# Optimization experiments

Hardware: AMD Instinct MI355X
Metric: run time of the kernel (lower is better)

The kernel has to match this reference:

```python
import jax, jax.numpy as jnp
import numpy as np

D = 1024  # input_size == context_size

def setup_inputs() -> dict:
    key = jax.random.key(0)
    ks = jax.random.split(key, 8)
    B, S = 16, 4096
    s = 1.0 / np.sqrt(D)
    return {
        "x": jax.random.normal(ks[0], (B, S, D), dtype=jnp.float32),
        "context": jax.random.normal(ks[1], (B, D), dtype=jnp.float32),
        "W_in": jax.random.uniform(ks[2], (D, D), jnp.float32, -s, s),
        "b_in": jax.random.uniform(ks[3], (D,), jnp.float32, -s, s),
        "W_ctx": jax.random.uniform(ks[4], (D, D), jnp.float32, -s, s),
        "b_ctx": jax.random.uniform(ks[5], (D,), jnp.float32, -s, s),
        "w_att": jax.random.uniform(ks[6], (D,), jnp.float32, -s, s),
        "b_att": jax.random.uniform(ks[7], (), jnp.float32, -s, s),
    }

def reference(x, context, W_in, b_in, W_ctx, b_ctx, w_att, b_att):
    # projected_input: [B,S,D]; projected_context: [B,D] broadcast over S
    pi = jnp.einsum('bsd,ed->bse', x, W_in) + b_in
    pc = jnp.einsum('bd,ed->be', context, W_ctx) + b_ctx
    h = jnp.tanh(pi + pc[:, None, :])                      # [B,S,D]
    scores = jnp.einsum('bsd,d->bs', h, w_att) + b_att      # [B,S]
    weights = jax.nn.softmax(scores, axis=1)                # [B,S]
    context_vector = jnp.einsum('bs,bsd->bd', weights, x)   # [B,D]
    # dropout is identity in eval mode
    return context_vector
```

## Files before the change

kernel.cpp:

```cpp
#include <hip/hip_runtime.h>
#include <hip/hip_bf16.h>
#include <math.h>

#define NB 16
#define NS 4096
#define ND 1024
#define NM (NB * NS)

#define WS_T       0
#define WS_SCORES  16384
#define WS_WEIGHTS (WS_SCORES + NB * NS)
#define WS_SHARED  (WS_WEIGHTS + NB * NS)
#define WS_XBF16   (WS_SHARED + 524288)
#define WS_SPART   (WS_XBF16 + 33554432)
#define WS_NEED    (((size_t)WS_SPART + 524288) * 4)

typedef short v8s __attribute__((ext_vector_type(8)));
typedef float v4f __attribute__((ext_vector_type(4)));
typedef unsigned short ushort;

#define G_AS __attribute__((address_space(1)))
#define L_AS __attribute__((address_space(3)))

__device__ __forceinline__ ushort f2bf(float f) {
    __hip_bfloat16 h = __float2bfloat16(f);
    return *reinterpret_cast<ushort*>(&h);
}

__device__ __forceinline__ float bf2f(ushort u) {
    return __uint_as_float(((unsigned)u) << 16);
}

__device__ __forceinline__ float fast_tanh(float x) {
    float e = __expf(2.0f * x);
    return 1.0f - 2.0f / (e + 1.0f);
}

__global__ __launch_bounds__(256) void convw_kernel(const float* __restrict__ W,
                                                    ushort* __restrict__ Wb) {
    int flat = blockIdx.x * 256 + threadIdx.x;
#pragma unroll
    for (int j = 0; j < 2; ++j) {
        int idx = flat + j * 131072;
        float4 v = ((const float4*)W)[idx];
        ushort4 o;
        o.x = f2bf(v.x); o.y = f2bf(v.y); o.z = f2bf(v.z); o.w = f2bf(v.w);
        ((ushort4*)Wb)[idx] = o;
    }
}

__global__ __launch_bounds__(256) void convx_kernel(const float* __restrict__ x,
                                                    ushort* __restrict__ xb) {
    size_t base = (size_t)blockIdx.x * 256 + threadIdx.x;
#pragma unroll
    for (int i = 0; i < 16; ++i) {
        size_t idx8 = base + (size_t)i * 524288;
        float4 a = ((const float4*)x)[idx8 * 2];
        float4 c = ((const float4*)x)[idx8 * 2 + 1];
        v8s o;
        o[0] = (short)f2bf(a.x); o[1] = (short)f2bf(a.y);
        o[2] = (short)f2bf(a.z); o[3] = (short)f2bf(a.w);
        o[4] = (short)f2bf(c.x); o[5] = (short)f2bf(c.y);
        o[6] = (short)f2bf(c.z); o[7] = (short)f2bf(c.w);
        ((v8s*)xb)[idx8] = o;
    }
}

__global__ __launch_bounds__(256) void tvec_kernel(const float* __restrict__ context,
                                                   const float* __restrict__ W_ctx,
                                                   const float* __restrict__ b_in,
                                                   const float* __restrict__ b_ctx,
                                                   float* __restrict__ t) {
    __shared__ float ctx[ND];
    int b = blockIdx.y;
    int tid = threadIdx.x;
    for (int i = tid; i < ND; i += 256) ctx[i] = context[b * ND + i];
    __syncthreads();
    int e = blockIdx.x * 64 + (tid >> 2);
    int kq = tid & 3;
    const float4* wr = (const float4*)(W_ctx + (size_t)e * ND + kq * 256);
    const float4* cr = (const float4*)(ctx + kq * 256);
    float acc = 0.f;
#pragma unroll 4
    for (int k = 0; k < 64; ++k) {
        float4 w = wr[k];
        float4 c = cr[k];
        acc += c.x * w.x + c.y * w.y + c.z * w.z + c.w * w.w;
    }
    acc += __shfl_xor(acc, 1);
    acc += __shfl_xor(acc, 2);
    if (kq == 0) t[b * ND + e] = acc + b_in[e] + b_ctx[e];
}

__global__ __launch_bounds__(256) void scores_tile_kernel(const ushort* __restrict__ xbf,
                                                          const ushort* __restrict__ Wb,
                                                          const float* __restrict__ t,
                                                          const float* __restrict__ w_att,
                                                          float* __restrict__ spart) {
    __shared__ ushort As[2][4096];
    __shared__ ushort Bs[2][4096];
    __shared__ float red[4][64];

    int tid = threadIdx.x;
    int o = blockIdx.x;
    int rt = (o & 7) * 64 + (o >> 6);
    int ct = (o >> 3) & 7;
    int row0 = rt << 7;
    int e0 = ct << 7;
    int b = row0 >> 12;

    int g0 = tid, g1 = tid + 256;
    const ushort* gaA0 = xbf + (size_t)(row0 + (g0 >> 2)) * ND + (g0 & 3) * 8;
    const ushort* gaA1 = xbf + (size_t)(row0 + (g1 >> 2)) * ND + (g1 & 3) * 8;
    const ushort* gaB0 = Wb  + (size_t)(e0  + (g0 >> 2)) * ND + (g0 & 3) * 8;
    const ushort* gaB1 = Wb  + (size_t)(e0  + (g1 >> 2)) * ND + (g1 & 3) * 8;

    __builtin_amdgcn_global_load_lds((const G_AS void*)gaA0, (L_AS void*)&As[0][g0 * 8], 16, 0, 0);
    __builtin_amdgcn_global_load_lds((const G_AS void*)gaA1, (L_AS void*)&As[0][g1 * 8], 16, 0, 0);
    __builtin_amdgcn_global_load_lds((const G_AS void*)gaB0, (L_AS void*)&Bs[0][g0 * 8], 16, 0, 0);
    __builtin_amdgcn_global_load_lds((const G_AS void*)gaB1, (L_AS void*)&Bs[0][g1 * 8], 16, 0, 0);
    __syncthreads();

    int w = tid >> 6, l = tid & 63;
    int l15 = l & 15, kq4 = l >> 4;
    int R = (w >> 1) * 64;
    int E = (w & 1) * 64;

    v4f acc[4][4];
#pragma unroll
    for (int i = 0; i < 4; ++i)
#pragma unroll
        for (int j = 0; j < 4; ++j) acc[i][j] = (v4f)(0.f);

#pragma unroll 2
    for (int kt = 0; kt < 32; ++kt) {
        int bi = kt & 1;
        if (kt < 31) {
            int ko = (kt + 1) * 32;
            __builtin_amdgcn_global_load_lds((const G_AS void*)(gaA0 + ko), (L_AS void*)&As[bi ^ 1][g0 * 8], 16, 0, 0);
            __builtin_amdgcn_global_load_lds((const G_AS void*)(gaA1 + ko), (L_AS void*)&As[bi ^ 1][g1 * 8], 16, 0, 0);
            __builtin_amdgcn_global_load_lds((const G_AS void*)(gaB0 + ko), (L_AS void*)&Bs[bi ^ 1][g0 * 8], 16, 0, 0);
            __builtin_amdgcn_global_load_lds((const G_AS void*)(gaB1 + ko), (L_AS void*)&Bs[bi ^ 1][g1 * 8], 16, 0, 0);
        }
        v8s af[4], bf[4];
#pragma unroll
        for (int mf = 0; mf < 4; ++mf)
            af[mf] = *(const v8s*)&As[bi][((R + mf * 16 + l15) * 4 + kq4) * 8];
#pragma unroll
        for (int nf = 0; nf < 4; ++nf)
            bf[nf] = *(const v8s*)&Bs[bi][((E + nf * 16 + l15) * 4 + kq4) * 8];
#pragma unroll
        for (int mf = 0; mf < 4; ++mf)
#pragma unroll
            for (int nf = 0; nf < 4; ++nf)
                acc[mf][nf] = __builtin_amdgcn_mfma_f32_16x16x32_bf16(
                    af[mf], bf[nf], acc[mf][nf], 0, 0, 0);
        __syncthreads();
    }

    float s[4][4];
#pragma unroll
    for (int i = 0; i < 4; ++i)
#pragma unroll
        for (int j = 0; j < 4; ++j) s[i][j] = 0.f;

#pragma unroll
    for (int nf = 0; nf < 4; ++nf) {
        int e = e0 + E + nf * 16 + l15;
        float tv = t[b * ND + e];
        float wv = w_att[e];
#pragma unroll
        for (int mf = 0; mf < 4; ++mf)
#pragma unroll
            for (int r = 0; r < 4; ++r)
                s[mf][r] += fast_tanh(acc[mf][nf][r] + tv) * wv;
    }
#pragma unroll
    for (int mf = 0; mf < 4; ++mf)
#pragma unroll
        for (int r = 0; r < 4; ++r) {
            float v = s[mf][r];
            v += __shfl_xor(v, 1);
            v += __shfl_xor(v, 2);
            v += __shfl_xor(v, 4);
            v += __shfl_xor(v, 8);
            s[mf][r] = v;
        }
    if (l15 == 0) {
#pragma unroll
        for (int mf = 0; mf < 4; ++mf)
#pragma unroll
            for (int r = 0; r < 4; ++r)
                red[w][mf * 16 + kq4 * 4 + r] = s[mf][r];
    }
    __syncthreads();
    if (tid < 128) {
        int half = tid >> 6;
        int rl = tid & 63;
        float v = red[half * 2][rl] + red[half * 2 + 1][rl];
        spart[ct * 65536 + row0 + half * 64 + rl] = v;
    }
}

__global__ __launch_bounds__(512) void scores_mfma_kernel(const float* __restrict__ x,
                                                          const ushort* __restrict__ Wb,
                                                          const float* __restrict__ t,
                                                          const float* __restrict__ w_att,
                                                          float* __restrict__ scores) {
    __shared__ ushort As[2][64 * 256];
    __shared__ float red[8][64];

    int tid = threadIdx.x;
    int row0 = blockIdx.x * 64;
    int b = row0 >> 12;
    const float4* xf4 = (const float4*)x;

    int sr = tid >> 3;
    int sc = tid & 7;
    int swzbase = (sr & 7) << 3;

    float4 nx[8];
#pragma unroll
    for (int j = 0; j < 8; ++j)
        nx[j] = xf4[(size_t)(row0 + sr) * 256 + sc + j * 8];
#pragma unroll
    for (int j = 0; j < 8; ++j) {
        int c4 = sc + j * 8;
        ushort4 o;
        o.x = f2bf(nx[j].x); o.y = f2bf(nx[j].y); o.z = f2bf(nx[j].z); o.w = f2bf(nx[j].w);
        *(ushort4*)&As[0][sr * 256 + ((c4 * 4) ^ swzbase)] = o;
    }
    __syncthreads();

    int w = tid >> 6;
    int l = tid & 63;
    int l15 = l & 15;
    int kofs = (l >> 4) * 8;
    int xorv = (l & 7) << 3;
    int n0 = w * 128;

    v4f acc[2][4][4];
#pragma unroll
    for (int p = 0; p < 2; ++p)
#pragma unroll
        for (int i = 0; i < 4; ++i)
#pragma unroll
            for (int j = 0; j < 4; ++j) acc[p][i][j] = (v4f)(0.f);

    const ushort* bbase0 = Wb + (size_t)(n0 + l15) * ND + kofs;
    const ushort* bbase1 = bbase0 + (size_t)64 * ND;

#pragma unroll
    for (int kh = 0; kh < 4; ++kh) {
        if (kh < 3) {
#pragma unroll
            for (int j = 0; j < 8; ++j)
                nx[j] = xf4[(size_t)(row0 + sr) * 256 + (kh + 1) * 64 + sc + j * 8];
        }
        const ushort* Ab = &As[kh & 1][0];
        int kb = kh * 256;

        v8s b0c[4], b0n[4], b1[4];
#pragma unroll
        for (int nf = 0; nf < 4; ++nf) b0c[nf] = *(const v8s*)(bbase0 + (size_t)nf * 16 * ND + kb);

#pragma unroll
        for (int ks = 0; ks < 8; ++ks) {
            int kk = kb + ks * 32;
            int elem = (ks * 32 + kofs) ^ xorv;
            v8s af[4];
#pragma unroll
            for (int mf = 0; mf < 4; ++mf)
                af[mf] = *(const v8s*)&Ab[(mf * 16 + l15) * 256 + elem];
#pragma unroll
            for (int nf = 0; nf < 4; ++nf)
                b1[nf] = *(const v8s*)(bbase1 + (size_t)nf * 16 * ND + kk);
            if (ks < 7) {
#pragma unroll
                for (int nf = 0; nf < 4; ++nf)
                    b0n[nf] = *(const v8s*)(bbase0 + (size_t)nf * 16 * ND + kk + 32);
            }
#pragma unroll
            for (int mf = 0; mf < 4; ++mf)
#pragma unroll
                for (int nf = 0; nf < 4; ++nf)
                    acc[0][mf][nf] = __builtin_amdgcn_mfma_f32_16x16x32_bf16(
                        af[mf], b0c[nf], acc[0][mf][nf], 0, 0, 0);
#pragma unroll
            for (int mf = 0; mf < 4; ++mf)
#pragma unroll
                for (int nf = 0; nf < 4; ++nf)
                    acc[1][mf][nf] = __builtin_amdgcn_mfma_f32_16x16x32_bf16(
                        af[mf], b1[nf], acc[1][mf][nf], 0, 0, 0);
#pragma unroll
            for (int nf = 0; nf < 4; ++nf) b0c[nf] = b0n[nf];
        }

        if (kh < 3) {
#pragma unroll
            for (int j = 0; j < 8; ++j) {
                int c4 = sc + j * 8;
                ushort4 o;
                o.x = f2bf(nx[j].x); o.y = f2bf(nx[j].y); o.z = f2bf(nx[j].z); o.w = f2bf(nx[j].w);
                *(ushort4*)&As[(kh + 1) & 1][sr * 256 + ((c4 * 4) ^ swzbase)] = o;
            }
            __syncthreads();
        }
    }

    float s[4][4];
#pragma unroll
    for (int i = 0; i < 4; ++i)
#pragma unroll
        for (int j = 0; j < 4; ++j) s[i][j] = 0.f;

#pragma unroll
    for (int pass = 0; pass < 2; ++pass)
#pragma unroll
        for (int nf = 0; nf < 4; ++nf) {
            int e = n0 + pass * 64 + nf * 16 + l15;
            float tv = t[b * ND + e];
            float wv = w_att[e];
#pragma unroll
            for (int mf = 0; mf < 4; ++mf)
#pragma unroll
                for (int r = 0; r < 4; ++r)
                    s[mf][r] += fast_tanh(acc[pass][mf][nf][r] + tv) * wv;
        }

#pragma unroll
    for (int mf = 0; mf < 4; ++mf)
#pragma unroll
        for (int r = 0; r < 4; ++r) {
            float v = s[mf][r];
            v += __shfl_xor(v, 1);
            v += __shfl_xor(v, 2);
            v += __shfl_xor(v, 4);
            v += __shfl_xor(v, 8);
            s[mf][r] = v;
        }
    if (l15 == 0) {
#pragma unroll
        for (int mf = 0; mf < 4; ++mf)
#pragma unroll
            for (int r = 0; r < 4; ++r)
                red[w][mf * 16 + (l >> 4) * 4 + r] = s[mf][r];
    }
    __syncthreads();
    if (tid < 64) {
        float v = 0.f;
#pragma unroll
        for (int ww = 0; ww < 8; ++ww) v += red[ww][tid];
        scores[(size_t)b * NS + (row0 & (NS - 1)) + tid] = v;
    }
}

__global__ __launch_bounds__(256) void softmax8_kernel(const float* __restrict__ spart,
                                                       float* __restrict__ weights) {
    int b = blockIdx.x;
    int tid = threadIdx.x;
    float v[16];
    float lmax = -1e30f;
#pragma unroll
    for (int i = 0; i < 16; ++i) {
        int grow = b * NS + tid + i * 256;
        float sum = 0.f;
#pragma unroll
        for (int c = 0; c < 8; ++c) sum += spart[c * 65536 + grow];
        v[i] = sum;
        lmax = fmaxf(lmax, sum);
    }
#pragma unroll
    for (int off = 32; off >= 1; off >>= 1) lmax = fmaxf(lmax, __shfl_xor(lmax, off));
    __shared__ float redm[4];
    int wave = tid >> 6;
    if ((tid & 63) == 0) redm[wave] = lmax;
    __syncthreads();
    float bmax = fmaxf(fmaxf(redm[0], redm[1]), fmaxf(redm[2], redm[3]));

    float lsum = 0.f;
#pragma unroll
    for (int i = 0; i < 16; ++i) {
        v[i] = expf(v[i] - bmax);
        lsum += v[i];
    }
#pragma unroll
    for (int off = 32; off >= 1; off >>= 1) lsum += __shfl_xor(lsum, off);
    __shared__ float reds[4];
    if ((tid & 63) == 0) reds[wave] = lsum;
    __syncthreads();
    float inv = 1.0f / (reds[0] + reds[1] + reds[2] + reds[3]);
#pragma unroll
    for (int i = 0; i < 16; ++i) weights[b * NS + tid + i * 256] = v[i] * inv;
}

__global__ __launch_bounds__(256) void softmax_kernel(const float* __restrict__ scores,
                                                      float* __restrict__ weights) {
    int b = blockIdx.x;
    int tid = threadIdx.x;
    float v[16];
    float lmax = -1e30f;
#pragma unroll
    for (int i = 0; i < 16; ++i) {
        v[i] = scores[b * NS + tid + i * 256];
        lmax = fmaxf(lmax, v[i]);
    }
#pragma unroll
    for (int off = 32; off >= 1; off >>= 1) lmax = fmaxf(lmax, __shfl_xor(lmax, off));
    __shared__ float redm[4];
    int wave = tid >> 6;
    if ((tid & 63) == 0) redm[wave] = lmax;
    __syncthreads();
    float bmax = fmaxf(fmaxf(redm[0], redm[1]), fmaxf(redm[2], redm[3]));

    float lsum = 0.f;
#pragma unroll
    for (int i = 0; i < 16; ++i) {
        v[i] = expf(v[i] - bmax);
        lsum += v[i];
    }
#pragma unroll
    for (int off = 32; off >= 1; off >>= 1) lsum += __shfl_xor(lsum, off);
    __shared__ float reds[4];
    if ((tid & 63) == 0) reds[wave] = lsum;
    __syncthreads();
    float inv = 1.0f / (reds[0] + reds[1] + reds[2] + reds[3]);
#pragma unroll
    for (int i = 0; i < 16; ++i) weights[b * NS + tid + i * 256] = v[i] * inv;
}

__global__ __launch_bounds__(256) void wsum_kernel(const float* __restrict__ x,
                                                   const float* __restrict__ w,
                                                   float* __restrict__ part) {
    int sc = blockIdx.x, b = blockIdx.y;
    int d0 = threadIdx.x * 4;
    const float* xb = x + ((size_t)b * NS + sc * 128) * ND;
    const float* wb = w + b * NS + sc * 128;
    float4 acc = {0.f, 0.f, 0.f, 0.f};
    for (int ss = 0; ss < 128; ++ss) {
        float wv = wb[ss];
        float4 xv = *(const float4*)&xb[(size_t)ss * ND + d0];
        acc.x += wv * xv.x;
        acc.y += wv * xv.y;
        acc.z += wv * xv.z;
        acc.w += wv * xv.w;
    }
    *(float4*)&part[(size_t)(b * 32 + sc) * ND + d0] = acc;
}

__global__ __launch_bounds__(256) void wsum_bf_kernel(const ushort* __restrict__ xbf,
                                                      const float* __restrict__ w,
                                                      float* __restrict__ part) {
    int sc = blockIdx.x, b = blockIdx.y;
    int d0 = threadIdx.x * 4;
    const ushort* xb = xbf + ((size_t)b * NS + sc * 128) * ND;
    const float* wb = w + b * NS + sc * 128;
    float4 acc = {0.f, 0.f, 0.f, 0.f};
    for (int ss = 0; ss < 128; ++ss) {
        float wv = wb[ss];
        ushort4 xv = *(const ushort4*)&xb[(size_t)ss * ND + d0];
        acc.x += wv * bf2f(xv.x);
        acc.y += wv * bf2f(xv.y);
        acc.z += wv * bf2f(xv.z);
        acc.w += wv * bf2f(xv.w);
    }
    *(float4*)&part[(size_t)(b * 32 + sc) * ND + d0] = acc;
}

__global__ __launch_bounds__(256) void reduce_kernel(const float* __restrict__ part,
                                                     float* __restrict__ out) {
    int b = blockIdx.x;
    int d0 = threadIdx.x * 4;
    float4 acc = {0.f, 0.f, 0.f, 0.f};
#pragma unroll
    for (int sc = 0; sc < 32; ++sc) {
        float4 v = *(const float4*)&part[(size_t)(b * 32 + sc) * ND + d0];
        acc.x += v.x;
        acc.y += v.y;
        acc.z += v.z;
        acc.w += v.w;
    }
    *(float4*)&out[b * ND + d0] = acc;
}

extern "C" void kernel_launch(void* const* d_in, const int* in_sizes, int n_in,
                              void* d_out, int out_size, void* d_ws, size_t ws_size,
                              hipStream_t stream) {
    const float* x       = (const float*)d_in[0];
    const float* context = (const float*)d_in[1];
    const float* W_in    = (const float*)d_in[2];
    const float* b_in    = (const float*)d_in[3];
    const float* W_ctx   = (const float*)d_in[4];
    const float* b_ctx   = (const float*)d_in[5];
    const float* w_att   = (const float*)d_in[6];

    float* ws      = (float*)d_ws;
    float* t       = ws + WS_T;
    float* scores  = ws + WS_SCORES;
    float* weights = ws + WS_WEIGHTS;
    ushort* wbf16  = (ushort*)(ws + WS_SHARED);
    ushort* xbf16  = (ushort*)(ws + WS_XBF16);
    float* spart   = ws + WS_SPART;
    float* partfb  = ws + WS_SHARED;
    float* out     = (float*)d_out;

    bool fast = ws_size >= WS_NEED;

    convw_kernel<<<dim3(512), 256, 0, stream>>>(W_in, wbf16);
    tvec_kernel<<<dim3(16, NB), 256, 0, stream>>>(context, W_ctx, b_in, b_ctx, t);
    if (fast) {
        convx_kernel<<<dim3(2048), 256, 0, stream>>>(x, xbf16);
        scores_tile_kernel<<<dim3(4096), 256, 0, stream>>>(xbf16, wbf16, t, w_att, spart);
        softmax8_kernel<<<dim3(NB), 256, 0, stream>>>(spart, weights);
        wsum_bf_kernel<<<dim3(32, NB), 256, 0, stream>>>(xbf16, weights, spart);
        reduce_kernel<<<dim3(NB), 256, 0, stream>>>(spart, out);
    } else {
        scores_mfma_kernel<<<dim3(NM / 64), 512, 0, stream>>>(x, wbf16, t, w_att, scores);
        softmax_kernel<<<dim3(NB), 256, 0, stream>>>(scores, weights);
        wsum_kernel<<<dim3(32, NB), 256, 0, stream>>>(x, weights, partfb);
        reduce_kernel<<<dim3(NB), 256, 0, stream>>>(partfb, out);
    }
}
```

Measured before the change: 314.7 us.

## Triple-buffer LDS tiles in scores GEMM with explicit vmcnt waits

The scores GEMM kernel moves from double to triple buffering of the A/B LDS tiles, keeping two K-steps of global_load_lds in flight. A raw s_waitcnt vmcnt with split barriers replaces the full __syncthreads that ended each iteration. The goal is to hide more global-memory latency behind the MFMA work. The cost is 50% more LDS per block, which may lower occupancy, and the hand-written vmcnt counts must match the issued loads exactly.

```diff
diff --git a/kernel.cpp b/kernel.cpp
--- a/kernel.cpp
+++ b/kernel.cpp
@@ -97,8 +97,8 @@
                                                           const float* __restrict__ t,
                                                           const float* __restrict__ w_att,
                                                           float* __restrict__ spart) {
-    __shared__ ushort As[2][4096];
-    __shared__ ushort Bs[2][4096];
+    __shared__ ushort As[3][4096];
+    __shared__ ushort Bs[3][4096];
     __shared__ float red[4][64];
 
     int tid = threadIdx.x;
@@ -115,12 +115,6 @@
     const ushort* gaB0 = Wb  + (size_t)(e0  + (g0 >> 2)) * ND + (g0 & 3) * 8;
     const ushort* gaB1 = Wb  + (size_t)(e0  + (g1 >> 2)) * ND + (g1 & 3) * 8;
 
-    __builtin_amdgcn_global_load_lds((const G_AS void*)gaA0, (L_AS void*)&As[0][g0 * 8], 16, 0, 0);
-    __builtin_amdgcn_global_load_lds((const G_AS void*)gaA1, (L_AS void*)&As[0][g1 * 8], 16, 0, 0);
-    __builtin_amdgcn_global_load_lds((const G_AS void*)gaB0, (L_AS void*)&Bs[0][g0 * 8], 16, 0, 0);
-    __builtin_amdgcn_global_load_lds((const G_AS void*)gaB1, (L_AS void*)&Bs[0][g1 * 8], 16, 0, 0);
-    __syncthreads();
-
     int w = tid >> 6, l = tid & 63;
     int l15 = l & 15, kq4 = l >> 4;
     int R = (w >> 1) * 64;
@@ -132,31 +126,59 @@
 #pragma unroll
         for (int j = 0; j < 4; ++j) acc[i][j] = (v4f)(0.f);
 
-#pragma unroll 2
-    for (int kt = 0; kt < 32; ++kt) {
-        int bi = kt & 1;
-        if (kt < 31) {
-            int ko = (kt + 1) * 32;
-            __builtin_amdgcn_global_load_lds((const G_AS void*)(gaA0 + ko), (L_AS void*)&As[bi ^ 1][g0 * 8], 16, 0, 0);
-            __builtin_amdgcn_global_load_lds((const G_AS void*)(gaA1 + ko), (L_AS void*)&As[bi ^ 1][g1 * 8], 16, 0, 0);
-            __builtin_amdgcn_global_load_lds((const G_AS void*)(gaB0 + ko), (L_AS void*)&Bs[bi ^ 1][g0 * 8], 16, 0, 0);
-            __builtin_amdgcn_global_load_lds((const G_AS void*)(gaB1 + ko), (L_AS void*)&Bs[bi ^ 1][g1 * 8], 16, 0, 0);
-        }
-        v8s af[4], bf[4];
-#pragma unroll
-        for (int mf = 0; mf < 4; ++mf)
-            af[mf] = *(const v8s*)&As[bi][((R + mf * 16 + l15) * 4 + kq4) * 8];
-#pragma unroll
-        for (int nf = 0; nf < 4; ++nf)
-            bf[nf] = *(const v8s*)&Bs[bi][((E + nf * 16 + l15) * 4 + kq4) * 8];
-#pragma unroll
-        for (int mf = 0; mf < 4; ++mf)
-#pragma unroll
-            for (int nf = 0; nf < 4; ++nf)
-                acc[mf][nf] = __builtin_amdgcn_mfma_f32_16x16x32_bf16(
-                    af[mf], bf[nf], acc[mf][nf], 0, 0, 0);
-        __syncthreads();
-    }
+#define STAGE(BUF, KO)                                                                                              \
+    {                                                                                                               \
+        __builtin_amdgcn_global_load_lds((const G_AS void*)(gaA0 + (KO)), (L_AS void*)&As[BUF][g0 * 8], 16, 0, 0);  \
+        __builtin_amdgcn_global_load_lds((const G_AS void*)(gaA1 + (KO)), (L_AS void*)&As[BUF][g1 * 8], 16, 0, 0);  \
+        __builtin_amdgcn_global_load_lds((const G_AS void*)(gaB0 + (KO)), (L_AS void*)&Bs[BUF][g0 * 8], 16, 0, 0);  \
+        __builtin_amdgcn_global_load_lds((const G_AS void*)(gaB1 + (KO)), (L_AS void*)&Bs[BUF][g1 * 8], 16, 0, 0);  \
+    }
+
+#define COMPUTE(BUF)                                                                          \
+    {                                                                                         \
+        v8s af[4], bf[4];                                                                     \
+        _Pragma("unroll") for (int mf = 0; mf < 4; ++mf)                                      \
+            af[mf] = *(const v8s*)&As[BUF][((R + mf * 16 + l15) * 4 + kq4) * 8];              \
+        _Pragma("unroll") for (int nf = 0; nf < 4; ++nf)                                      \
+            bf[nf] = *(const v8s*)&Bs[BUF][((E + nf * 16 + l15) * 4 + kq4) * 8];              \
+        _Pragma("unroll") for (int mf = 0; mf < 4; ++mf)                                      \
+            _Pragma("unroll") for (int nf = 0; nf < 4; ++nf)                                  \
+                acc[mf][nf] = __builtin_amdgcn_mfma_f32_16x16x32_bf16(af[mf], bf[nf],         \
+                                                                      acc[mf][nf], 0, 0, 0);  \
+    }
+
+#define KSTEP(KT, BUF, STBUF, VMTOK)                                 \
+    {                                                                \
+        __builtin_amdgcn_s_barrier();                                \
+        STAGE(STBUF, ((KT) + 2) * 32);                               \
+        asm volatile("s_waitcnt vmcnt(" VMTOK ")" ::: "memory");     \
+        __builtin_amdgcn_s_barrier();                                \
+        asm volatile("" ::: "memory");                               \
+        COMPUTE(BUF);                                                \
+    }
+
+    STAGE(0, 0);
+    STAGE(1, 32);
+
+    for (int tt = 0; tt < 10; ++tt) {
+        KSTEP(3 * tt + 0, 0, 2, "8");
+        KSTEP(3 * tt + 1, 1, 0, "8");
+        KSTEP(3 * tt + 2, 2, 1, "8");
+    }
+    __builtin_amdgcn_s_barrier();
+    asm volatile("s_waitcnt vmcnt(4)" ::: "memory");
+    __builtin_amdgcn_s_barrier();
+    asm volatile("" ::: "memory");
+    COMPUTE(0);
+    __builtin_amdgcn_s_barrier();
+    asm volatile("s_waitcnt vmcnt(0)" ::: "memory");
+    __builtin_amdgcn_s_barrier();
+    asm volatile("" ::: "memory");
+    COMPUTE(1);
+
+#undef KSTEP
+#undef COMPUTE
+#undef STAGE
 
     float s[4][4];
 #pragma unroll
```

Result: no change. 319.3 us (+1.5%).
